# Kernel tuning notes

Measured on AMD Instinct MI355X. Metric: run time of the kernel, lower is better.

## Reference

```python
import jax, jax.numpy as jnp
import numpy as np
from jax import lax

BOS, EOS = 1, 2
MAX_LEN = 16
BEAM = 4
VOCAB = 32000
INF = 1e9


def _gather_beams(x, idx):
    # x: [B, K, ...] or [B, K]; idx: [B, k]
    if x.ndim == 3:
        return jnp.take_along_axis(x, idx[:, :, None], axis=1)
    return jnp.take_along_axis(x, idx, axis=1)


def setup_inputs() -> dict:
    key = jax.random.key(0)
    k1, k2, k3, k4 = jax.random.split(key, 4)
    B, S, D = 16, 128, 512
    return {
        "src_input": jax.random.randint(k1, (B, S), 0, VOCAB),
        "E_src": jax.random.normal(k2, (VOCAB, D), jnp.float32) * 0.02,
        "E_tgt": jax.random.normal(k3, (VOCAB, D), jnp.float32) * 0.02,
        "W": jax.random.normal(k4, (D, VOCAB), jnp.float32) * 0.02,
        "b": jnp.zeros((VOCAB,), jnp.float32),
    }


def _beam_search(src_input, E_src, E_tgt, W, b):
    B = src_input.shape[0]
    # tile_by_beam: repeat each batch row beam_size times
    src = jnp.repeat(src_input, BEAM, axis=0)                     # [B*BEAM, S]
    # stub encoder: embedding + masked mean pool (pad token = 0)
    enc = E_src[src]                                              # [B*BEAM, S, D]
    keep = (src != 0).astype(enc.dtype)[..., None]
    pooled = (enc * keep).sum(1) / jnp.maximum(keep.sum(1), 1.0)  # [B*BEAM, D]

    alive_seq = jnp.zeros((B, BEAM, MAX_LEN), jnp.int32).at[:, :, 0].set(BOS)
    alive_lp = jnp.full((B, BEAM), -jnp.inf, jnp.float32).at[:, 0].set(0.0)
    fin_seq = jnp.zeros((B, BEAM, MAX_LEN), jnp.int32)
    fin_scores = jnp.full((B, BEAM), -INF, jnp.float32)
    fin_flags = jnp.zeros((B, BEAM), bool)
    batch_fin = jnp.zeros((B,), bool)
    batch_idx = jnp.arange(B)[:, None]

    for t in range(MAX_LEN - 1):
        # stub decoder: last-token embedding + encoder summary -> vocab logits
        last = alive_seq[:, :, t].reshape(B * BEAM)
        logits = (E_tgt[last] + pooled) @ W + b                   # [B*BEAM, V]
        lp = jax.nn.log_softmax(logits, axis=-1).reshape(B, BEAM, VOCAB)
        log_probs = alive_lp[:, :, None] + lp                     # [B, BEAM, V]
        lpen = jnp.float32(t + 1)
        flat = (log_probs / lpen).reshape(B, BEAM * VOCAB)
        topk_scores, topk_ids = lax.top_k(flat, BEAM * 2)         # [B, 2*BEAM]
        topk_lp = topk_scores * lpen
        if t == 0:
            beam_idx = jnp.tile(jnp.arange(BEAM), (B, 2))
        else:
            beam_idx = topk_ids // VOCAB
        tok = topk_ids % VOCAB
        topk_seq = alive_seq[batch_idx, beam_idx]                 # [B, 2*BEAM, L]
        topk_seq = topk_seq.at[:, :, t + 1].set(tok.astype(jnp.int32))
        topk_fin = tok == EOS
        # alive set: penalize finished candidates
        curr = topk_scores + topk_fin.astype(jnp.float32) * -INF
        _, a_idx = lax.top_k(curr, BEAM)
        alive_seq = _gather_beams(topk_seq, a_idx)
        alive_lp = _gather_beams(topk_lp, a_idx)
        # finished set: penalize unfinished + already-finished batches
        fs = (topk_scores + (1.0 - topk_fin.astype(jnp.float32)) * -INF
              + batch_fin[:, None].astype(jnp.float32) * -INF)
        cand_seq = jnp.concatenate([fin_seq, topk_seq], axis=1)   # [B, 3*BEAM, L]
        cand_sc = jnp.concatenate([fin_scores, fs], axis=1)
        cand_fl = jnp.concatenate([fin_flags, topk_fin], axis=1)
        _, f_idx = lax.top_k(cand_sc, BEAM)
        fin_seq = _gather_beams(cand_seq, f_idx)
        fin_scores = _gather_beams(cand_sc, f_idx)
        fin_flags = _gather_beams(cand_fl, f_idx)
        # batch-finished lower-bound test
        lb_alive = alive_lp[:, 0] / lpen
        lowest_fin = jnp.min(fin_scores * fin_flags.astype(jnp.float32), axis=1)
        lowest_fin = lowest_fin + (1.0 - jnp.all(fin_flags, axis=1).astype(jnp.float32)) * -INF
        batch_fin = batch_fin | (lowest_fin >= lb_alive)
    return fin_seq, fin_scores


def reference(src_input, E_src, E_tgt, W, b):
    fin_seq, _ = _beam_search(src_input, E_src, E_tgt, W, b)
    return fin_seq[:, 0]  # one_best_output [B, MAX_LEN] int32
```

## Files before the change

### kernel.cpp

```cpp
#include <hip/hip_runtime.h>
#include <math.h>

#define BATCH 16
#define SRCLEN 128
#define DIM 512
#define VOCABSZ 32000
#define BEAM 4
#define MAXLEN 16
#define NROWS (BATCH*BEAM)
#define BOS_TOK 1
#define EOS_TOK 2
#define NEGINF 1e9f
#define CHUNKS 8
#define CHUNK 4000
#define PCH 8
#define PCL (SRCLEN/PCH)

__device__ inline unsigned long long packkey(float v, int idx) {
    unsigned int fb = __float_as_uint(v);
    fb = fb ^ ((fb >> 31) ? 0xFFFFFFFFu : 0x80000000u);
    return ((unsigned long long)fb << 32) | (unsigned long long)(0xFFFFFFFFu - (unsigned int)idx);
}
__device__ inline float unpack_val(unsigned long long k) {
    unsigned int fb = (unsigned int)(k >> 32);
    fb = fb ^ ((fb >> 31) ? 0x80000000u : 0xFFFFFFFFu);
    return __uint_as_float(fb);
}
__device__ inline int unpack_id(unsigned long long k) {
    return (int)(0xFFFFFFFFu - (unsigned int)(k & 0xFFFFFFFFu));
}
__device__ inline unsigned long long shflxor64(unsigned long long x, int mask) {
    unsigned int lo = (unsigned int)x, hi = (unsigned int)(x >> 32);
    lo = (unsigned int)__shfl_xor((int)lo, mask, 64);
    hi = (unsigned int)__shfl_xor((int)hi, mask, 64);
    return ((unsigned long long)hi << 32) | (unsigned long long)lo;
}
__device__ inline unsigned long long wavemax64(unsigned long long k) {
#pragma unroll
    for (int off = 1; off < 64; off <<= 1) {
        unsigned long long o = shflxor64(k, off);
        k = (o > k) ? o : k;
    }
    return k;
}

__global__ __launch_bounds__(512) void k_pool2(const int* __restrict__ src,
                                               const float* __restrict__ Esrc,
                                               float* __restrict__ pp, float* __restrict__ pcnt) {
    int b = blockIdx.x, c = blockIdx.y;
    int d = threadIdx.x;
    float acc = 0.f, cnt = 0.f;
#pragma unroll
    for (int s = 0; s < PCL; ++s) {
        int tok = src[b * SRCLEN + c * PCL + s];
        if (tok != 0) { acc += Esrc[(size_t)tok * DIM + d]; cnt += 1.f; }
    }
    pp[(b * PCH + c) * DIM + d] = acc;
    if (d == 0) pcnt[b * PCH + c] = cnt;
}

__global__ __launch_bounds__(512) void k_poolred(const float* __restrict__ pp,
                                                 const float* __restrict__ pcnt,
                                                 float* __restrict__ pooled) {
    int b = blockIdx.x;
    int d = threadIdx.x;
    float acc = 0.f, cnt = 0.f;
#pragma unroll
    for (int c = 0; c < PCH; ++c) { acc += pp[(b * PCH + c) * DIM + d]; cnt += pcnt[b * PCH + c]; }
    pooled[b * DIM + d] = acc / fmaxf(cnt, 1.f);
}

__global__ __launch_bounds__(1024) void k_init(int* __restrict__ alive_seq, float* __restrict__ alive_lp,
                                               int* __restrict__ fin_seq, float* __restrict__ fin_scores,
                                               int* __restrict__ fin_flags, int* __restrict__ batch_fin) {
    int tid = threadIdx.x;
    alive_seq[tid] = (tid % MAXLEN == 0) ? BOS_TOK : 0;
    fin_seq[tid] = 0;
    if (tid < NROWS) {
        alive_lp[tid] = (tid % BEAM == 0) ? 0.f : -INFINITY;
        fin_scores[tid] = -NEGINF;
        fin_flags[tid] = 0;
    }
    if (tid < BATCH) batch_fin[tid] = 0;
}

__global__ __launch_bounds__(512) void k_x(const float* __restrict__ Etgt,
                                           const float* __restrict__ pooled,
                                           const int* __restrict__ alive_seq, int t,
                                           float* __restrict__ xT) {
    int i = blockIdx.x;
    int d = threadIdx.x;
    int last = alive_seq[i * MAXLEN + t];
    float v = Etgt[(size_t)last * DIM + d] + pooled[(i >> 2) * DIM + d];
    xT[d * NROWS + i] = v;
}

#define FMA4(i, xs, wq) \
    acc[i].x = fmaf((xs),(wq).x,acc[i].x); acc[i].y = fmaf((xs),(wq).y,acc[i].y); \
    acc[i].z = fmaf((xs),(wq).z,acc[i].z); acc[i].w = fmaf((xs),(wq).w,acc[i].w);
#define FMAD_LDS(wq, dd) { \
    float4 xa = *(const float4*)(xsp + (dd) * NROWS);      \
    float4 xb = *(const float4*)(xsp + (dd) * NROWS + 4);  \
    float4 xc = *(const float4*)(xsp + (dd) * NROWS + 8);  \
    float4 xd = *(const float4*)(xsp + (dd) * NROWS + 12); \
    FMA4(0, xa.x, wq)  FMA4(1, xa.y, wq)  FMA4(2, xa.z, wq)  FMA4(3, xa.w, wq)  \
    FMA4(4, xb.x, wq)  FMA4(5, xb.y, wq)  FMA4(6, xb.z, wq)  FMA4(7, xb.w, wq)  \
    FMA4(8, xc.x, wq)  FMA4(9, xc.y, wq)  FMA4(10, xc.z, wq) FMA4(11, xc.w, wq) \
    FMA4(12, xd.x, wq) FMA4(13, xd.y, wq) FMA4(14, xd.z, wq) FMA4(15, xd.w, wq) }
#define LOADW(P, dbase) \
    w##P##0 = *(const float4*)(wp + (size_t)((dbase)+0) * VOCABSZ); \
    w##P##1 = *(const float4*)(wp + (size_t)((dbase)+1) * VOCABSZ); \
    w##P##2 = *(const float4*)(wp + (size_t)((dbase)+2) * VOCABSZ); \
    w##P##3 = *(const float4*)(wp + (size_t)((dbase)+3) * VOCABSZ);
#define FMACHUNK(P, dbase) \
    FMAD_LDS(w##P##0, (dbase)+0) FMAD_LDS(w##P##1, (dbase)+1) \
    FMAD_LDS(w##P##2, (dbase)+2) FMAD_LDS(w##P##3, (dbase)+3)

template<int GDLEN>
__global__ __launch_bounds__(256) void k_gemm9(const float* __restrict__ xT,
                                               const float* __restrict__ W,
                                               float* __restrict__ partial) {
    int lane = threadIdx.x & 63;
    int r0 = __builtin_amdgcn_readfirstlane((threadIdx.x >> 6) * 16);
    int v0 = blockIdx.x * 256 + lane * 4;
    int z  = blockIdx.z;
    int d0 = z * GDLEN;

    __shared__ float xs[GDLEN * NROWS];
    {
        const float4* xg = (const float4*)(xT + (size_t)d0 * NROWS);
        float4* xs4 = (float4*)xs;
#pragma unroll
        for (int i = 0; i < (GDLEN * NROWS / 4) / 256; ++i)
            xs4[i * 256 + threadIdx.x] = xg[i * 256 + threadIdx.x];
    }
    __syncthreads();

    float4 acc[16];
#pragma unroll
    for (int i = 0; i < 16; ++i) acc[i] = make_float4(0.f, 0.f, 0.f, 0.f);

    const float* wp  = W + (size_t)d0 * VOCABSZ + v0;
    const float* xsp = xs + r0;
    float4 wA0, wA1, wA2, wA3, wB0, wB1, wB2, wB3;

    const int nc = GDLEN / 4;
    LOADW(A, 0)
    for (int c = 0; c < nc; c += 2) {
        LOADW(B, (c + 1) * 4)
        FMACHUNK(A, c * 4)
        if (c + 2 < nc) { LOADW(A, (c + 2) * 4) }
        FMACHUNK(B, (c + 1) * 4)
    }

    float* op = partial + (size_t)z * NROWS * VOCABSZ + (size_t)r0 * VOCABSZ + v0;
#pragma unroll
    for (int r = 0; r < 16; ++r)
        *(float4*)(op + (size_t)r * VOCABSZ) = acc[r];
}

template<int NZ>
__global__ __launch_bounds__(1024) void k_part(const float* __restrict__ partial,
                                               const float* __restrict__ bias,
                                               float* __restrict__ pm, float* __restrict__ ps,
                                               float* __restrict__ ptopv, int* __restrict__ ptopi) {
    int row = blockIdx.x, ch = blockIdx.y;
    int tid = threadIdx.x;
    int lane = tid & 63;
    int wv = tid >> 6;
    const size_t slab = (size_t)NROWS * VOCABSZ;
    const bool valid = tid < (CHUNK / 4);

    float vals[4] = {-INFINITY, -INFINITY, -INFINITY, -INFINITY};
    if (valid) {
        const float4* l0 = (const float4*)(partial + (size_t)row * VOCABSZ + ch * CHUNK);
        float4 q = l0[tid];
#pragma unroll
        for (int zz = 1; zz < NZ; ++zz) {
            const float4* lz = (const float4*)(partial + slab * zz + (size_t)row * VOCABSZ + ch * CHUNK);
            float4 q2 = lz[tid];
            q.x += q2.x; q.y += q2.y; q.z += q2.z; q.w += q2.w;
        }
        float4 bb = ((const float4*)(bias + ch * CHUNK))[tid];
        vals[0] = q.x + bb.x; vals[1] = q.y + bb.y; vals[2] = q.z + bb.z; vals[3] = q.w + bb.w;
    }

    float m_t = fmaxf(fmaxf(vals[0], vals[1]), fmaxf(vals[2], vals[3]));
#pragma unroll
    for (int off = 1; off < 64; off <<= 1) m_t = fmaxf(m_t, __shfl_xor(m_t, off, 64));
    __shared__ float swred[16];
    if (lane == 0) swred[wv] = m_t;
    __syncthreads();
    float m = swred[0];
#pragma unroll
    for (int w = 1; w < 16; ++w) m = fmaxf(m, swred[w]);
    __syncthreads();

    float se = 0.f;
    if (valid) {
#pragma unroll
        for (int c = 0; c < 4; ++c) se += expf(vals[c] - m);
    }
#pragma unroll
    for (int off = 1; off < 64; off <<= 1) se += __shfl_xor(se, off, 64);
    if (lane == 0) swred[wv] = se;
    __syncthreads();
    if (tid == 0) {
        float s = 0.f;
#pragma unroll
        for (int w = 0; w < 16; ++w) s += swred[w];
        pm[row * CHUNKS + ch] = m;
        ps[row * CHUNKS + ch] = s;
    }

    int gi = ch * CHUNK + tid * 4;
    unsigned long long k0 = 0ULL, k1 = 0ULL, k2 = 0ULL, k3 = 0ULL;
    if (valid) {
        k0 = packkey(vals[0], gi);
        k1 = packkey(vals[1], gi + 1);
        k2 = packkey(vals[2], gi + 2);
        k3 = packkey(vals[3], gi + 3);
    }
    {
        unsigned long long tswp;
#define CSW(a,b) if (b > a) { tswp = a; a = b; b = tswp; }
        CSW(k0,k1) CSW(k2,k3) CSW(k0,k2) CSW(k1,k3) CSW(k1,k2)
#undef CSW
    }
    __shared__ unsigned long long skey[128];
    {
        int pos = 0;
        unsigned long long wtop[8];
#pragma unroll
        for (int r = 0; r < 8; ++r) {
            unsigned long long head = (pos == 0) ? k0 : (pos == 1) ? k1 :
                                      (pos == 2) ? k2 : (pos == 3) ? k3 : 0ULL;
            unsigned long long mx = wavemax64(head);
            if (head == mx && head != 0ULL) pos++;
            wtop[r] = mx;
        }
        if (lane == 0) {
#pragma unroll
            for (int r = 0; r < 8; ++r) skey[wv * 8 + r] = wtop[r];
        }
    }
    __syncthreads();
    if (tid < 64) {
        unsigned long long a = skey[tid];
        unsigned long long b2 = skey[64 + tid];
        unsigned long long hi = (a > b2) ? a : b2;
        unsigned long long lo = (a > b2) ? b2 : a;
        float* otv = ptopv + ((size_t)row * CHUNKS + ch) * 8;
        int*   oti = ptopi + ((size_t)row * CHUNKS + ch) * 8;
        int pos = 0;
#pragma unroll
        for (int r = 0; r < 8; ++r) {
            unsigned long long head = (pos == 0) ? hi : (pos == 1) ? lo : 0ULL;
            unsigned long long mx = wavemax64(head);
            if (head == mx && head != 0ULL) pos++;
            if (tid == 0) { otv[r] = unpack_val(mx); oti[r] = unpack_id(mx); }
        }
    }
}

__global__ __launch_bounds__(64) void k_mergesel(const float* __restrict__ pm, const float* __restrict__ ps,
                                                 const float* __restrict__ ptopv, const int* __restrict__ ptopi,
                                                 int* __restrict__ alive_seq, float* __restrict__ alive_lp,
                                                 int* __restrict__ fin_seq, float* __restrict__ fin_scores,
                                                 int* __restrict__ fin_flags, int* __restrict__ batch_fin, int t) {
    int b = blockIdx.x;
    int tid = threadIdx.x;
    __shared__ int aseq_old[BEAM][MAXLEN]; __shared__ int fseq_old[BEAM][MAXLEN];
    __shared__ float s_tlp[8]; __shared__ int s_ttok[8], s_tbeam[8];
    __shared__ int s_aidx[4], s_fidx[4];
    __shared__ float s_nfsc[4]; __shared__ int s_nffl[4];
    float lpen = (float)(t + 1);

    { int k = tid >> 4, p = tid & 15;
      aseq_old[k][p] = alive_seq[(b * BEAM + k) * MAXLEN + p];
      fseq_old[k][p] = fin_seq[(b * BEAM + k) * MAXLEN + p]; }

    float rv[4]; int ri[4];
#pragma unroll
    for (int k = 0; k < 4; ++k) {
        rv[k] = ptopv[(size_t)(b * BEAM + k) * 64 + tid];
        ri[k] = ptopi[(size_t)(b * BEAM + k) * 64 + tid];
    }

    float alp[4], fsc[4]; int ffl[4];
#pragma unroll
    for (int k = 0; k < 4; ++k) {
        alp[k] = alive_lp[b * BEAM + k];
        fsc[k] = fin_scores[b * BEAM + k];
        ffl[k] = fin_flags[b * BEAM + k];
    }
    int bf_old = batch_fin[b];

    float srm[4], srl[4];
#pragma unroll
    for (int k = 0; k < 4; ++k) {
        float m = -INFINITY;
#pragma unroll
        for (int c = 0; c < CHUNKS; ++c) m = fmaxf(m, pm[(b * BEAM + k) * CHUNKS + c]);
        float s = 0.f;
#pragma unroll
        for (int c = 0; c < CHUNKS; ++c) s += ps[(b * BEAM + k) * CHUNKS + c] * expf(pm[(b * BEAM + k) * CHUNKS + c] - m);
        srm[k] = m; srl[k] = logf(s);
    }

    unsigned long long key[4];
#pragma unroll
    for (int k = 0; k < 4; ++k) {
        float sh = rv[k] - srm[k];
        float lp = sh - srl[k];
        float full = alp[k] + lp;
        float cv = full / lpen;
        key[k] = packkey(cv, k * VOCABSZ + ri[k]);
    }
    {
        unsigned long long tmp;
#define CSW(a,b) if (key[b] > key[a]) { tmp = key[a]; key[a] = key[b]; key[b] = tmp; }
        CSW(0,1) CSW(2,3) CSW(0,2) CSW(1,3) CSW(1,2)
#undef CSW
    }

    float tscore[8], tlp[8]; int ttok[8], tbeam[8], tfin[8];
    int pos = 0;
#pragma unroll
    for (int r = 0; r < 8; ++r) {
        unsigned long long head = (pos == 0) ? key[0] : (pos == 1) ? key[1] :
                                  (pos == 2) ? key[2] : (pos == 3) ? key[3] : 0ULL;
        unsigned long long mx = wavemax64(head);
        if (head == mx && head != 0ULL) pos++;
        float sc = unpack_val(mx);
        int id = unpack_id(mx);
        tscore[r] = sc;
        tlp[r] = sc * lpen;
        ttok[r] = id % VOCABSZ;
        tbeam[r] = id / VOCABSZ;
        tfin[r] = (ttok[r] == EOS_TOK) ? 1 : 0;
    }

    int aidx[4];
    {
        float curr[8];
#pragma unroll
        for (int j = 0; j < 8; ++j) curr[j] = tscore[j] + (tfin[j] ? -NEGINF : 0.0f);
        unsigned int used = 0;
#pragma unroll
        for (int r = 0; r < 4; ++r) {
            float bv = 0.f; int bj = -1;
#pragma unroll
            for (int j = 0; j < 8; ++j) {
                bool skip = (used >> j) & 1u;
                bool better = !skip && (bj < 0 || curr[j] > bv);
                if (better) { bv = curr[j]; bj = j; }
            }
            used |= 1u << bj; aidx[r] = bj;
        }
    }
    int fidx[4]; float nfsc[4]; int nffl[4];
    {
        float fscand[12]; int fflcand[12];
#pragma unroll
        for (int j = 0; j < 4; ++j) { fscand[j] = fsc[j]; fflcand[j] = ffl[j]; }
#pragma unroll
        for (int q = 0; q < 8; ++q) {
            float t1 = tscore[q] + (tfin[q] ? 0.0f : -NEGINF);
            float t2 = t1 + (bf_old ? -NEGINF : 0.0f);
            fscand[4 + q] = t2; fflcand[4 + q] = tfin[q];
        }
        unsigned int used = 0;
#pragma unroll
        for (int r = 0; r < 4; ++r) {
            float bv = 0.f; int bj = -1;
#pragma unroll
            for (int j = 0; j < 12; ++j) {
                bool skip = (used >> j) & 1u;
                bool better = !skip && (bj < 0 || fscand[j] > bv);
                if (better) { bv = fscand[j]; bj = j; }
            }
            used |= 1u << bj; fidx[r] = bj;
            nfsc[r] = bv;
        }
#pragma unroll
        for (int r = 0; r < 4; ++r) {
            int bj = fidx[r]; int fl = 0;
#pragma unroll
            for (int j = 0; j < 12; ++j) if (bj == j) fl = fflcand[j];
            nffl[r] = fl;
        }
    }

    if (tid == 0) {
#pragma unroll
        for (int r = 0; r < 8; ++r) { s_tlp[r] = tlp[r]; s_ttok[r] = ttok[r]; s_tbeam[r] = tbeam[r]; }
#pragma unroll
        for (int r = 0; r < 4; ++r) { s_aidx[r] = aidx[r]; s_fidx[r] = fidx[r]; s_nfsc[r] = nfsc[r]; s_nffl[r] = nffl[r]; }
    }
    __syncthreads();

    { int k = tid >> 4, p = tid & 15;
      int j = s_aidx[k];
      int val = (p == t + 1) ? s_ttok[j] : aseq_old[s_tbeam[j]][p];
      alive_seq[(b * BEAM + k) * MAXLEN + p] = val;
      int fi = s_fidx[k]; int fval;
      if (fi < 4) fval = fseq_old[fi][p];
      else { int q = fi - 4; fval = (p == t + 1) ? s_ttok[q] : aseq_old[s_tbeam[q]][p]; }
      fin_seq[(b * BEAM + k) * MAXLEN + p] = fval; }

    if (tid < 4) {
        alive_lp[b * BEAM + tid] = s_tlp[s_aidx[tid]];
        fin_scores[b * BEAM + tid] = s_nfsc[tid];
        fin_flags[b * BEAM + tid] = s_nffl[tid];
    }
    if (tid == 0) {
        float lb = s_tlp[s_aidx[0]] / lpen;
        float lowest = nfsc[0] * (nffl[0] ? 1.f : 0.f);
        int allf = nffl[0];
#pragma unroll
        for (int k2 = 1; k2 < 4; ++k2) {
            float pz = nfsc[k2] * (nffl[k2] ? 1.f : 0.f);
            lowest = fminf(lowest, pz);
            allf = allf && nffl[k2];
        }
        lowest = lowest + (allf ? 0.f : -NEGINF);
        batch_fin[b] = bf_old || (lowest >= lb);
    }
}

__global__ __launch_bounds__(256) void k_out(const int* __restrict__ fin_seq, float* __restrict__ out) {
    int tid = threadIdx.x;
    if (tid < BATCH * MAXLEN) {
        int b = tid / MAXLEN, p = tid % MAXLEN;
        out[tid] = (float)fin_seq[(b * BEAM + 0) * MAXLEN + p];
    }
}

extern "C" void kernel_launch(void* const* d_in, const int* in_sizes, int n_in,
                              void* d_out, int out_size, void* d_ws, size_t ws_size,
                              hipStream_t stream) {
    const int*   src  = (const int*)d_in[0];
    const float* Esrc = (const float*)d_in[1];
    const float* Etgt = (const float*)d_in[2];
    const float* W    = (const float*)d_in[3];
    const float* bias = (const float*)d_in[4];
    float* out = (float*)d_out;

    const size_t slab = (size_t)NROWS * VOCABSZ * 4;
    const bool big4 = ws_size >= 4 * slab + (2u << 20);
    const int NZ = big4 ? 4 : 2;

    char* p = (char*)d_ws;
    float* partial    = (float*)p; p += NZ * slab;
    float* pooled     = (float*)p; p += BATCH * DIM * 4;
    float* xT         = (float*)p; p += DIM * NROWS * 4;
    float* pp         = (float*)p; p += BATCH * PCH * DIM * 4;
    float* pcnt       = (float*)p; p += BATCH * PCH * 4;
    float* pm         = (float*)p; p += NROWS * CHUNKS * 4;
    float* ps         = (float*)p; p += NROWS * CHUNKS * 4;
    float* ptopv      = (float*)p; p += NROWS * CHUNKS * 8 * 4;
    int*   ptopi      = (int*)p;   p += NROWS * CHUNKS * 8 * 4;
    int*   alive_seq  = (int*)p;   p += NROWS * MAXLEN * 4;
    int*   fin_seq    = (int*)p;   p += NROWS * MAXLEN * 4;
    float* alive_lp   = (float*)p; p += NROWS * 4;
    float* fin_scores = (float*)p; p += NROWS * 4;
    int*   fin_flags  = (int*)p;   p += NROWS * 4;
    int*   batch_fin  = (int*)p;   p += BATCH * 4;

    k_pool2<<<dim3(BATCH, PCH), DIM, 0, stream>>>(src, Esrc, pp, pcnt);
    k_poolred<<<BATCH, DIM, 0, stream>>>(pp, pcnt, pooled);
    k_init<<<1, 1024, 0, stream>>>(alive_seq, alive_lp, fin_seq, fin_scores, fin_flags, batch_fin);
    for (int t = 0; t < MAXLEN - 1; ++t) {
        k_x<<<NROWS, DIM, 0, stream>>>(Etgt, pooled, alive_seq, t, xT);
        if (big4) {
            k_gemm9<DIM/4><<<dim3(VOCABSZ / 256, 1, 4), 256, 0, stream>>>(xT, W, partial);
            k_part<4><<<dim3(NROWS, CHUNKS), 1024, 0, stream>>>(partial, bias, pm, ps, ptopv, ptopi);
        } else {
            k_gemm9<DIM/2><<<dim3(VOCABSZ / 256, 1, 2), 256, 0, stream>>>(xT, W, partial);
            k_part<2><<<dim3(NROWS, CHUNKS), 1024, 0, stream>>>(partial, bias, pm, ps, ptopv, ptopi);
        }
        k_mergesel<<<BATCH, 64, 0, stream>>>(pm, ps, ptopv, ptopi, alive_seq, alive_lp,
                                             fin_seq, fin_scores, fin_flags, batch_fin, t);
    }
    k_out<<<1, 256, 0, stream>>>(fin_seq, out);
}
```

Baseline: 1.078 ms.

## Widen GEMM register tile to 8 vocab columns and add 8-way K split

```diff
diff --git a/kernel.cpp b/kernel.cpp
--- a/kernel.cpp
+++ b/kernel.cpp
@@ -95,34 +95,36 @@
     xT[d * NROWS + i] = v;
 }
 
-#define FMA4(i, xs, wq) \
-    acc[i].x = fmaf((xs),(wq).x,acc[i].x); acc[i].y = fmaf((xs),(wq).y,acc[i].y); \
-    acc[i].z = fmaf((xs),(wq).z,acc[i].z); acc[i].w = fmaf((xs),(wq).w,acc[i].w);
-#define FMAD_LDS(wq, dd) { \
+#define FMA8(i, xsc, wqa, wqb) \
+    acc[2*(i)].x   = fmaf((xsc),(wqa).x,acc[2*(i)].x);   acc[2*(i)].y   = fmaf((xsc),(wqa).y,acc[2*(i)].y); \
+    acc[2*(i)].z   = fmaf((xsc),(wqa).z,acc[2*(i)].z);   acc[2*(i)].w   = fmaf((xsc),(wqa).w,acc[2*(i)].w); \
+    acc[2*(i)+1].x = fmaf((xsc),(wqb).x,acc[2*(i)+1].x); acc[2*(i)+1].y = fmaf((xsc),(wqb).y,acc[2*(i)+1].y); \
+    acc[2*(i)+1].z = fmaf((xsc),(wqb).z,acc[2*(i)+1].z); acc[2*(i)+1].w = fmaf((xsc),(wqb).w,acc[2*(i)+1].w);
+#define FMAD2(wqa, wqb, dd) { \
     float4 xa = *(const float4*)(xsp + (dd) * NROWS);      \
     float4 xb = *(const float4*)(xsp + (dd) * NROWS + 4);  \
     float4 xc = *(const float4*)(xsp + (dd) * NROWS + 8);  \
     float4 xd = *(const float4*)(xsp + (dd) * NROWS + 12); \
-    FMA4(0, xa.x, wq)  FMA4(1, xa.y, wq)  FMA4(2, xa.z, wq)  FMA4(3, xa.w, wq)  \
-    FMA4(4, xb.x, wq)  FMA4(5, xb.y, wq)  FMA4(6, xb.z, wq)  FMA4(7, xb.w, wq)  \
-    FMA4(8, xc.x, wq)  FMA4(9, xc.y, wq)  FMA4(10, xc.z, wq) FMA4(11, xc.w, wq) \
-    FMA4(12, xd.x, wq) FMA4(13, xd.y, wq) FMA4(14, xd.z, wq) FMA4(15, xd.w, wq) }
-#define LOADW(P, dbase) \
-    w##P##0 = *(const float4*)(wp + (size_t)((dbase)+0) * VOCABSZ); \
-    w##P##1 = *(const float4*)(wp + (size_t)((dbase)+1) * VOCABSZ); \
-    w##P##2 = *(const float4*)(wp + (size_t)((dbase)+2) * VOCABSZ); \
-    w##P##3 = *(const float4*)(wp + (size_t)((dbase)+3) * VOCABSZ);
-#define FMACHUNK(P, dbase) \
-    FMAD_LDS(w##P##0, (dbase)+0) FMAD_LDS(w##P##1, (dbase)+1) \
-    FMAD_LDS(w##P##2, (dbase)+2) FMAD_LDS(w##P##3, (dbase)+3)
+    FMA8(0,  xa.x, wqa, wqb) FMA8(1,  xa.y, wqa, wqb) FMA8(2,  xa.z, wqa, wqb) FMA8(3,  xa.w, wqa, wqb) \
+    FMA8(4,  xb.x, wqa, wqb) FMA8(5,  xb.y, wqa, wqb) FMA8(6,  xb.z, wqa, wqb) FMA8(7,  xb.w, wqa, wqb) \
+    FMA8(8,  xc.x, wqa, wqb) FMA8(9,  xc.y, wqa, wqb) FMA8(10, xc.z, wqa, wqb) FMA8(11, xc.w, wqa, wqb) \
+    FMA8(12, xd.x, wqa, wqb) FMA8(13, xd.y, wqa, wqb) FMA8(14, xd.z, wqa, wqb) FMA8(15, xd.w, wqa, wqb) }
+#define LOADW2(P, dbase) \
+    w##P##0 = *(const float4*)(wp + (size_t)((dbase)+0) * VOCABSZ);     \
+    w##P##1 = *(const float4*)(wp + (size_t)((dbase)+0) * VOCABSZ + 4); \
+    w##P##2 = *(const float4*)(wp + (size_t)((dbase)+1) * VOCABSZ);     \
+    w##P##3 = *(const float4*)(wp + (size_t)((dbase)+1) * VOCABSZ + 4);
+#define FMACHUNK2(P, dbase) \
+    FMAD2(w##P##0, w##P##1, (dbase)+0) FMAD2(w##P##2, w##P##3, (dbase)+1)
 
 template<int GDLEN>
-__global__ __launch_bounds__(256) void k_gemm9(const float* __restrict__ xT,
-                                               const float* __restrict__ W,
-                                               float* __restrict__ partial) {
+__global__ __launch_bounds__(256) void k_gemm10(const float* __restrict__ xT,
+                                                const float* __restrict__ W,
+                                                float* __restrict__ partial) {
     int lane = threadIdx.x & 63;
     int r0 = __builtin_amdgcn_readfirstlane((threadIdx.x >> 6) * 16);
-    int v0 = blockIdx.x * 256 + lane * 4;
+    int v0 = blockIdx.x * 512 + lane * 8;
+    if (v0 > VOCABSZ - 8) v0 = VOCABSZ - 8;
     int z  = blockIdx.z;
     int d0 = z * GDLEN;
 
@@ -136,27 +138,29 @@
     }
     __syncthreads();
 
-    float4 acc[16];
-#pragma unroll
-    for (int i = 0; i < 16; ++i) acc[i] = make_float4(0.f, 0.f, 0.f, 0.f);
+    float4 acc[32];
+#pragma unroll
+    for (int i = 0; i < 32; ++i) acc[i] = make_float4(0.f, 0.f, 0.f, 0.f);
 
     const float* wp  = W + (size_t)d0 * VOCABSZ + v0;
     const float* xsp = xs + r0;
     float4 wA0, wA1, wA2, wA3, wB0, wB1, wB2, wB3;
 
-    const int nc = GDLEN / 4;
-    LOADW(A, 0)
+    const int nc = GDLEN / 2;
+    LOADW2(A, 0)
     for (int c = 0; c < nc; c += 2) {
-        LOADW(B, (c + 1) * 4)
-        FMACHUNK(A, c * 4)
-        if (c + 2 < nc) { LOADW(A, (c + 2) * 4) }
-        FMACHUNK(B, (c + 1) * 4)
+        LOADW2(B, (c + 1) * 2)
+        FMACHUNK2(A, c * 2)
+        if (c + 2 < nc) { LOADW2(A, (c + 2) * 2) }
+        FMACHUNK2(B, (c + 1) * 2)
     }
 
     float* op = partial + (size_t)z * NROWS * VOCABSZ + (size_t)r0 * VOCABSZ + v0;
 #pragma unroll
-    for (int r = 0; r < 16; ++r)
-        *(float4*)(op + (size_t)r * VOCABSZ) = acc[r];
+    for (int r = 0; r < 16; ++r) {
+        *(float4*)(op + (size_t)r * VOCABSZ)     = acc[2*r];
+        *(float4*)(op + (size_t)r * VOCABSZ + 4) = acc[2*r+1];
+    }
 }
 
 template<int NZ>
@@ -448,8 +452,9 @@
     float* out = (float*)d_out;
 
     const size_t slab = (size_t)NROWS * VOCABSZ * 4;
+    const bool big8 = ws_size >= 8 * slab + (2u << 20);
     const bool big4 = ws_size >= 4 * slab + (2u << 20);
-    const int NZ = big4 ? 4 : 2;
+    const int NZ = big8 ? 8 : (big4 ? 4 : 2);
 
     char* p = (char*)d_ws;
     float* partial    = (float*)p; p += NZ * slab;
@@ -473,11 +478,14 @@
     k_init<<<1, 1024, 0, stream>>>(alive_seq, alive_lp, fin_seq, fin_scores, fin_flags, batch_fin);
     for (int t = 0; t < MAXLEN - 1; ++t) {
         k_x<<<NROWS, DIM, 0, stream>>>(Etgt, pooled, alive_seq, t, xT);
-        if (big4) {
-            k_gemm9<DIM/4><<<dim3(VOCABSZ / 256, 1, 4), 256, 0, stream>>>(xT, W, partial);
+        if (big8) {
+            k_gemm10<DIM/8><<<dim3(63, 1, 8), 256, 0, stream>>>(xT, W, partial);
+            k_part<8><<<dim3(NROWS, CHUNKS), 1024, 0, stream>>>(partial, bias, pm, ps, ptopv, ptopi);
+        } else if (big4) {
+            k_gemm10<DIM/4><<<dim3(63, 1, 4), 256, 0, stream>>>(xT, W, partial);
             k_part<4><<<dim3(NROWS, CHUNKS), 1024, 0, stream>>>(partial, bias, pm, ps, ptopv, ptopi);
         } else {
-            k_gemm9<DIM/2><<<dim3(VOCABSZ / 256, 1, 2), 256, 0, stream>>>(xT, W, partial);
+            k_gemm10<DIM/2><<<dim3(63, 1, 2), 256, 0, stream>>>(xT, W, partial);
             k_part<2><<<dim3(NROWS, CHUNKS), 1024, 0, stream>>>(partial, bias, pm, ps, ptopv, ptopi);
         }
         k_mergesel<<<BATCH, 64, 0, stream>>>(pm, ps, ptopv, ptopi, alive_seq, alive_lp,
```

Result: slower. 1.218 ms (+13.0%).
